# Performance work log

Measured on AMD Instinct MI355X. Metric: run time of the kernel, lower is better.

The kernel has to match this reference:

```python
import jax, jax.numpy as jnp
import numpy as np

B, SEG, DIM = 8, 16, 1024  # H = W = D = SEG is forced by the Linear(dim, dim) on H*S etc.
HID = DIM // 4


def setup_inputs() -> dict:
    key = jax.random.key(0)
    ks = jax.random.split(key, 16)
    def lin(k, i, o):
        return jax.random.normal(k, (i, o), jnp.float32) * 0.02
    return {
        "x": jax.random.normal(ks[0], (B, SEG, SEG, SEG, DIM), jnp.float32),
        "wh": lin(ks[1], DIM, DIM), "bh": jnp.zeros((DIM,), jnp.float32),
        "ww": lin(ks[2], DIM, DIM), "bw": jnp.zeros((DIM,), jnp.float32),
        "wd": lin(ks[3], DIM, DIM), "bd": jnp.zeros((DIM,), jnp.float32),
        "wc": lin(ks[4], DIM, DIM), "bc": jnp.zeros((DIM,), jnp.float32),
        "w1": lin(ks[5], DIM, HID), "b1": jnp.zeros((HID,), jnp.float32),
        "w2": lin(ks[6], HID, 4 * DIM), "b2": jnp.zeros((4 * DIM,), jnp.float32),
        "wp": lin(ks[7], DIM, DIM), "bp": jnp.zeros((DIM,), jnp.float32),
    }


def reference(x, wh, bh, ww, bw, wd, bd, wc, bc, w1, b1, w2, b2, wp, bp):
    Bn, H, Wn, D, C = x.shape
    seg = SEG
    S = C // seg
    xr = x.reshape(Bn, H, Wn, D, seg, S)

    # h-branch: mix along H axis (H*S == C)
    h = xr.transpose(0, 4, 2, 3, 1, 5).reshape(Bn, seg, Wn, D, H * S)
    h = (h @ wh + bh).reshape(Bn, seg, Wn, D, H, S).transpose(0, 4, 2, 3, 1, 5).reshape(Bn, H, Wn, D, C)

    # w-branch: mix along W axis
    w = xr.transpose(0, 1, 4, 3, 2, 5).reshape(Bn, H, seg, D, Wn * S)
    w = (w @ ww + bw).reshape(Bn, H, seg, D, Wn, S).transpose(0, 1, 4, 3, 2, 5).reshape(Bn, H, Wn, D, C)

    # d-branch: mix along D axis
    d = xr.transpose(0, 1, 2, 4, 3, 5).reshape(Bn, H, Wn, seg, D * S)
    d = (d @ wd + bd).reshape(Bn, H, Wn, seg, D, S).transpose(0, 1, 2, 4, 3, 5).reshape(Bn, H, Wn, D, C)

    # c-branch: plain channel mixing
    c = x @ wc + bc

    # reweight gate: global-average-pool then small MLP -> softmax over the 4 branches
    a = (h + w + d + c).mean(axis=(1, 2, 3))                 # (B, C)
    a = jax.nn.gelu(a @ w1 + b1, approximate=False) @ w2 + b2  # (B, 4C)
    a = jax.nn.softmax(a.reshape(Bn, C, 4).transpose(2, 0, 1), axis=0)  # (4, B, C)
    a = a[:, :, None, None, None, :]                          # (4, B, 1, 1, 1, C)

    out = h * a[0] + w * a[1] + d * a[2] + c * a[3]
    return out @ wp + bp
```

## Files before the change

kernel.cpp:

```cpp
#include <hip/hip_runtime.h>
#include <cstdint>
#include <cstddef>

typedef unsigned short u16;
typedef __attribute__((ext_vector_type(8))) __bf16 bf16x8;
typedef __attribute__((ext_vector_type(4))) float f32x4;
typedef __attribute__((ext_vector_type(4))) unsigned int u32x4;

__device__ __forceinline__ float bf2f(u16 u){
  union { unsigned int i; float f; } x; x.i = ((unsigned int)u) << 16; return x.f;
}
__device__ __forceinline__ u16 f2bf(float f){
  union { float f; unsigned int i; } x; x.f = f;
  unsigned int i = x.i;
  return (u16)((i + 0x7fffu + ((i >> 16) & 1u)) >> 16);
}
__device__ __forceinline__ void load_lds16(const u16* g, u16* l){
  __builtin_amdgcn_global_load_lds((const __attribute__((address_space(1))) void*)g,
                                   (__attribute__((address_space(3))) void*)l, 16, 0, 0);
}

__global__ __launch_bounds__(256) void k_transpose(
    const float* __restrict__ wh, const float* __restrict__ ww,
    const float* __restrict__ wd, const float* __restrict__ wc,
    const float* __restrict__ wp, u16* __restrict__ wT)
{
  __shared__ u16 tile[32][33];
  const float* src = (blockIdx.z==0)?wh:(blockIdx.z==1)?ww:(blockIdx.z==2)?wd:(blockIdx.z==3)?wc:wp;
  u16* dst = wT + (size_t)blockIdx.z * 1048576;
  int x = blockIdx.x*32 + threadIdx.x;
  int y0 = blockIdx.y*32;
  for (int i = threadIdx.y; i < 32; i += 8)
    tile[i][threadIdx.x] = f2bf(src[(size_t)(y0+i)*1024 + x]);
  __syncthreads();
  int x2 = y0 + threadIdx.x;
  int y2 = blockIdx.x*32;
  for (int i = threadIdx.y; i < 32; i += 8)
    dst[(size_t)(y2+i)*1024 + x2] = tile[threadIdx.x][i];
}

__global__ __launch_bounds__(256) void k_psum(
    const float* __restrict__ x, u16* __restrict__ xbf, float* __restrict__ P_h,
    float* __restrict__ PwP, float* __restrict__ PdP)
{
  const int b = blockIdx.x, cs = blockIdx.y, hg = blockIdx.z;
  const int th = threadIdx.x >> 7, tc = threadIdx.x & 127;
  const int h = hg*2 + th, c = cs*128 + tc;
  const size_t base = ((size_t)b<<22) + ((size_t)h<<18) + c;
  const float* xb = x + base;
  u16* xo = xbf + base;
  float sh = 0.f;
  float aW[16] = {}, aD[16] = {};
#pragma unroll
  for (int w = 0; w < 16; ++w)
#pragma unroll
    for (int d = 0; d < 16; ++d){
      float v = xb[(w<<14) + (d<<10)];
      xo[(w<<14) + (d<<10)] = f2bf(v);
      sh += v; aW[w] += v; aD[d] += v;
    }
  P_h[(size_t)((b<<4)+h)*1024 + c] = sh;
  const int part = hg*2 + th;
  float* pw = PwP + ((size_t)part<<17) + ((size_t)b<<14) + c;
  float* pd = PdP + ((size_t)part<<17) + ((size_t)b<<14) + c;
#pragma unroll
  for (int w = 0; w < 16; ++w) pw[w<<10] = aW[w];
#pragma unroll
  for (int d = 0; d < 16; ++d) pd[d<<10] = aD[d];
}

__global__ __launch_bounds__(256) void k_psum2(
    const float* __restrict__ PwP, const float* __restrict__ PdP,
    float* __restrict__ P_w, float* __restrict__ P_d)
{
  int idx = blockIdx.x*256 + threadIdx.x;
  float s = 0.f, t = 0.f;
#pragma unroll
  for (int p = 0; p < 16; ++p){ s += PwP[(size_t)p*131072 + idx]; t += PdP[(size_t)p*131072 + idx]; }
  P_w[idx] = s; P_d[idx] = t;
}

__global__ __launch_bounds__(256) void k_wred(
    const float* __restrict__ wh, const float* __restrict__ ww, const float* __restrict__ wd,
    float* __restrict__ wred)
{
  const float* src = (blockIdx.y==0)?wh:(blockIdx.y==1)?ww:wd;
  int idx = blockIdx.x*256 + threadIdx.x;
  int k = idx >> 6, S = idx & 63;
  float s = 0.f;
#pragma unroll
  for (int i = 0; i < 16; ++i) s += src[(size_t)k*1024 + i*64 + S];
  wred[(size_t)blockIdx.y*65536 + idx] = s;
}

__global__ __launch_bounds__(256) void k_asum(
    const float* __restrict__ P_h, const float* __restrict__ P_w, const float* __restrict__ P_d,
    const float* __restrict__ wred, const float* __restrict__ wc,
    const float* __restrict__ bhv, const float* __restrict__ bwv,
    const float* __restrict__ bdv, const float* __restrict__ bcv,
    float* __restrict__ a_sum)
{
  const int b = blockIdx.x, cs = blockIdx.y, tid = threadIdx.x;
  const int tc = tid & 127, ti = tid >> 7;
  const int c = cs*128 + tc, sg = c >> 6, S = c & 63;
  __shared__ float xbar[1024];
  __shared__ float red[2][128];
  for (int k = tid; k < 1024; k += 256){
    float s = 0.f;
#pragma unroll
    for (int hh = 0; hh < 16; ++hh) s += P_h[(size_t)(b*16+hh)*1024 + k];
    xbar[k] = s;
  }
  __syncthreads();
  const float* Ph = P_h + (size_t)b*16384;
  const float* Pw = P_w + (size_t)b*16384;
  const float* Pd = P_d + (size_t)b*16384;
  const float* whr = wred, *wwr = wred + 65536, *wdr = wred + 131072;
  float acc = 0.f;
  for (int i = ti*8; i < ti*8 + 8; ++i){
#pragma unroll 8
    for (int si = 0; si < 64; ++si){
      int k = i*64 + si;
      acc += Ph[i*1024 + sg*64 + si] * whr[(size_t)k*64 + S]
           + Pw[i*1024 + sg*64 + si] * wwr[(size_t)k*64 + S]
           + Pd[i*1024 + sg*64 + si] * wdr[(size_t)k*64 + S];
    }
  }
#pragma unroll 8
  for (int k = ti*512; k < ti*512 + 512; ++k) acc += xbar[k] * wc[(size_t)k*1024 + c];
  red[ti][tc] = acc;
  __syncthreads();
  if (ti == 0){
    float bs = 0.f;
#pragma unroll
    for (int i = 0; i < 16; ++i) bs += bhv[i*64+S] + bwv[i*64+S] + bdv[i*64+S];
    a_sum[b*1024 + c] = red[0][tc] + red[1][tc] + 4096.f*bcv[c] + 256.f*bs;
  }
}

__global__ __launch_bounds__(256) void k_mlp1(
    const float* __restrict__ a_sum, const float* __restrict__ w1,
    const float* __restrict__ b1, float* __restrict__ z1g)
{
  const int b = blockIdx.x, tid = threadIdx.x;
  __shared__ float af[1024];
  for (int i = tid; i < 1024; i += 256) af[i] = a_sum[b*1024 + i] * (1.0f/4096.0f);
  __syncthreads();
  float acc = b1[tid];
#pragma unroll 8
  for (int k = 0; k < 1024; ++k) acc += af[k] * w1[(size_t)k*256 + tid];
  z1g[b*256 + tid] = 0.5f * acc * (1.0f + erff(acc * 0.70710678118654752f));
}

__global__ __launch_bounds__(128) void k_mlp2(
    const float* __restrict__ z1g, const float* __restrict__ w2,
    const float* __restrict__ b2, float* __restrict__ alpha)
{
  const int b = blockIdx.x, js = blockIdx.y, tid = threadIdx.x;
  __shared__ float z1[256];
  z1[tid] = z1g[b*256 + tid];
  z1[tid+128] = z1g[b*256 + tid + 128];
  __syncthreads();
  const int cch = js*128 + tid;
  const int j0 = cch*4;
  f32x4 acc = *(const f32x4*)(b2 + j0);
#pragma unroll 8
  for (int k = 0; k < 256; ++k){
    f32x4 wv4 = *(const f32x4*)(w2 + (size_t)k*4096 + j0);
    float z = z1[k];
    acc[0] += z*wv4[0]; acc[1] += z*wv4[1]; acc[2] += z*wv4[2]; acc[3] += z*wv4[3];
  }
  float m = fmaxf(fmaxf(acc[0], acc[1]), fmaxf(acc[2], acc[3]));
  float e0 = expf(acc[0]-m), e1 = expf(acc[1]-m), e2 = expf(acc[2]-m), e3 = expf(acc[3]-m);
  float inv = 1.0f / (e0+e1+e2+e3);
  alpha[0*8192 + b*1024 + cch] = e0*inv;
  alpha[1*8192 + b*1024 + cch] = e1*inv;
  alpha[2*8192 + b*1024 + cch] = e2*inv;
  alpha[3*8192 + b*1024 + cch] = e3*inv;
}


#define STAGE_A(buf, kk, kt) \
  load_lds16(gA0 + (size_t)(kt)*strideK + (kk)*32, sA + (buf)*16384 + (kk)*8192); \
  load_lds16(gA1 + (size_t)(kt)*strideK + (kk)*32, sA + (buf)*16384 + (kk)*8192 + 4096)
#define STAGE_B(buf, kk, kt) \
  load_lds16(gB0 + (kt)*64 + (kk)*32, sB + (buf)*16384 + (kk)*8192); \
  load_lds16(gB1 + (kt)*64 + (kk)*32, sB + (buf)*16384 + (kk)*8192 + 4096)

#define PHASE(h, kk, buf, STAGE_STMT, VM) do{ \
  const u16* ar_ = ldsA + (buf)*16384 + (kk)*8192 + ardoff + (h)*2048; \
  const u16* br_ = ldsB + (buf)*16384 + (kk)*8192 + brdoff; \
  bf16x8 af_[4], bf_[4]; \
  _Pragma("unroll") for (int m_ = 0; m_ < 4; ++m_) af_[m_] = *(const bf16x8*)(ar_ + m_*512); \
  _Pragma("unroll") for (int n_ = 0; n_ < 4; ++n_) bf_[n_] = *(const bf16x8*)(br_ + n_*512); \
  STAGE_STMT; \
  if (VM) asm volatile("s_waitcnt vmcnt(4)" ::: "memory"); \
  __builtin_amdgcn_s_barrier(); \
  asm volatile("s_waitcnt lgkmcnt(0)" ::: "memory"); \
  __builtin_amdgcn_sched_barrier(0); \
  __builtin_amdgcn_s_setprio(1); \
  _Pragma("unroll") for (int m_ = 0; m_ < 4; ++m_) \
    _Pragma("unroll") for (int n_ = 0; n_ < 4; ++n_) \
      acc[(h)*4+m_][n_] = __builtin_amdgcn_mfma_f32_16x16x32_bf16(af_[m_], bf_[n_], acc[(h)*4+m_][n_], 0, 0, 0); \
  __builtin_amdgcn_s_setprio(0); \
  __builtin_amdgcn_s_barrier(); \
}while(0)

#define GEMM_PROLOGUE() do{ \
  load_lds16(gA0, sA);                 load_lds16(gA1, sA + 4096); \
  load_lds16(gB0, sB);                 load_lds16(gB1, sB + 4096); \
  load_lds16(gA0 + 32, sA + 8192);     load_lds16(gA1 + 32, sA + 8192 + 4096); \
  load_lds16(gB0 + 32, sB + 8192);     load_lds16(gB1 + 32, sB + 8192 + 4096); \
  load_lds16(gA0 + strideK, sA + 16384);   load_lds16(gA1 + strideK, sA + 16384 + 4096); \
  load_lds16(gB0 + 64, sB + 16384);        load_lds16(gB1 + 64, sB + 16384 + 4096); \
  asm volatile("s_waitcnt vmcnt(4)" ::: "memory"); \
  __builtin_amdgcn_s_barrier(); \
}while(0)

#define GEMM_MAINLOOP() \
  for (int i = 0; i < 8; ++i){ \
    const int t1 = 2*i + 1; \
    const int t2 = (2*i + 2 < 16) ? 2*i + 2 : 15; \
    const int t3 = (2*i + 3 < 16) ? 2*i + 3 : 15; \
    PHASE(0,0,0, STAGE_A(1,1,t1), 0); \
    PHASE(1,0,0, STAGE_B(1,1,t1), 0); \
    PHASE(0,1,0, STAGE_A(0,0,t2), 0); \
    PHASE(1,1,0, STAGE_B(0,0,t2), 1); \
    PHASE(0,0,1, STAGE_A(0,1,t2), 0); \
    PHASE(1,0,1, STAGE_B(0,1,t2), 0); \
    PHASE(0,1,1, STAGE_A(1,0,t3), 0); \
    PHASE(1,1,1, STAGE_B(1,0,t3), 1); \
  }

__global__ __launch_bounds__(512, 2) void k_branch_gemm(
    const u16* __restrict__ xbf, const u16* __restrict__ wT,
    const float* __restrict__ bh, const float* __restrict__ bw,
    const float* __restrict__ bd, const float* __restrict__ bc,
    u16* __restrict__ hbuf, u16* __restrict__ wbuf,
    u16* __restrict__ dbuf, u16* __restrict__ cbuf)
{
  const int p = blockIdx.x;
  const int id = (p & 7) * 256 + (p >> 3);
  const int ntile  = id & 3;
  const int rtile  = (id >> 2) & 127;
  const int branch = id >> 9;

  const int tid = threadIdx.x;
  const int wv = tid >> 6, l = tid & 63;

  __shared__ __align__(16) u16 ldsA[32768];
  __shared__ __align__(16) u16 ldsB[32768];

  const u16* wsel = wT + (size_t)branch * 1048576;
  const float* bias = (branch==0)?bh:(branch==1)?bw:(branch==2)?bd:bc;
  u16* obuf         = (branch==0)?hbuf:(branch==1)?wbuf:(branch==2)?dbuf:cbuf;

  const int lr = l >> 2;
  const int qg = ((l & 3) ^ ((lr >> 1) & 3)) * 8;
  int strideK;
  size_t cb0, cb1;
  {
    const int q1 = rtile & 15, b_ = rtile >> 4;
    const size_t q2a = wv, q2b = wv + 8;
    if (branch == 0){
      cb0 = ((size_t)b_<<22) + (q2a<<14) + ((size_t)q1<<6);
      cb1 = ((size_t)b_<<22) + (q2b<<14) + ((size_t)q1<<6);
      strideK = 262144;
    } else if (branch == 1){
      cb0 = ((size_t)b_<<22) + ((size_t)q1<<18) + (q2a<<6);
      cb1 = ((size_t)b_<<22) + ((size_t)q1<<18) + (q2b<<6);
      strideK = 16384;
    } else if (branch == 2){
      cb0 = ((size_t)b_<<22) + ((size_t)q1<<18) + (q2a<<14);
      cb1 = ((size_t)b_<<22) + ((size_t)q1<<18) + (q2b<<14);
      strideK = 1024;
    } else {
      size_t r0 = (size_t)(rtile*256 + wv*16);
      cb0 = r0 << 10; cb1 = (r0 + 128) << 10;
      strideK = 64;
    }
  }
  const int rsh = (branch == 2) ? 6 : 10;
  const u16* gA0 = xbf + cb0 + ((size_t)lr << rsh) + qg;
  const u16* gA1 = xbf + cb1 + ((size_t)lr << rsh) + qg;
  const u16* gB0 = wsel + (size_t)(ntile*256 + wv*16 + lr) * 1024 + qg;
  const u16* gB1 = gB0 + 128*1024;
  u16* sA = ldsA + wv*512;
  u16* sB = ldsB + wv*512;

  const int wm = wv >> 2, wn = wv & 3;
  const int fr = l & 15;
  const int cswz = ((l >> 4) ^ ((fr >> 1) & 3)) * 8;
  const int ardoff = (wm*128 + fr)*32 + cswz;
  const int brdoff = (wn*64  + fr)*32 + cswz;
  f32x4 acc[8][4] = {};

  GEMM_PROLOGUE();
  GEMM_MAINLOOP();

  const int bb_ = rtile >> 4, p1 = rtile & 15;
  int sc, s1, s2, s3;
  if      (branch==0){ sc=18; s1=6;  s2=14; s3=10; }
  else if (branch==1){ sc=14; s1=18; s2=6;  s3=10; }
  else if (branch==2){ sc=10; s1=18; s2=14; s3=6;  }
  else               { sc=6;  s1=18; s2=14; s3=10; }
#pragma unroll
  for (int mg = 0; mg < 8; ++mg){
    const int p2 = wm*8 + mg;
#pragma unroll
    for (int nf = 0; nf < 4; ++nf){
      int col = ntile*256 + wn*64 + nf*16 + fr;
      int ch = col >> 6, cl = col & 63;
      float bv = bias[col];
      size_t base = ((size_t)bb_<<22) | ((size_t)p1<<s1) | ((size_t)ch<<sc)
                  | ((size_t)p2<<s2) | (size_t)cl;
#pragma unroll
      for (int rg = 0; rg < 4; ++rg){
        int p3 = (l>>4)*4 + rg;
        obuf[base + ((size_t)p3<<s3)] = f2bf(acc[mg][nf][rg] + bv);
      }
    }
  }
}

__global__ __launch_bounds__(256) void k_mix(
    const u16* __restrict__ hbuf, const u16* __restrict__ wbuf,
    const u16* __restrict__ dbuf, const u16* __restrict__ cbuf,
    u16* __restrict__ mix, const float* __restrict__ alpha)
{
  int idx = blockIdx.x*256 + threadIdx.x;
  int p  = idx >> 7;
  int c0 = (idx & 127) << 3;
  int b = p >> 12;
  size_t off = ((size_t)p << 10) + c0;
  union { u32x4 v; u16 u[8]; } hv, wv, dv, cv, mv;
  hv.v = *(const u32x4*)(hbuf + off);
  wv.v = *(const u32x4*)(wbuf + off);
  dv.v = *(const u32x4*)(dbuf + off);
  cv.v = *(const u32x4*)(cbuf + off);
  union { f32x4 f[2]; float a[8]; } a0, a1, a2, a3;
  const float* ab = alpha + b*1024 + c0;
  a0.f[0] = *(const f32x4*)(ab);         a0.f[1] = *(const f32x4*)(ab + 4);
  a1.f[0] = *(const f32x4*)(ab + 8192);  a1.f[1] = *(const f32x4*)(ab + 8196);
  a2.f[0] = *(const f32x4*)(ab + 16384); a2.f[1] = *(const f32x4*)(ab + 16388);
  a3.f[0] = *(const f32x4*)(ab + 24576); a3.f[1] = *(const f32x4*)(ab + 24580);
#pragma unroll
  for (int e = 0; e < 8; ++e){
    float m = a0.a[e]*bf2f(hv.u[e]) + a1.a[e]*bf2f(wv.u[e])
            + a2.a[e]*bf2f(dv.u[e]) + a3.a[e]*bf2f(cv.u[e]);
    mv.u[e] = f2bf(m);
  }
  *(u32x4*)(mix + off) = mv.v;
}

__global__ __launch_bounds__(512, 2) void k_final_gemm(
    const u16* __restrict__ A, const u16* __restrict__ wpT,
    const float* __restrict__ bp, float* __restrict__ out)
{
  const int p = blockIdx.x;
  const int id = (p & 7) * 64 + (p >> 3);
  const int ntile = id & 3;
  const int rtile = id >> 2;

  const int tid = threadIdx.x;
  const int wv = tid >> 6, l = tid & 63;

  __shared__ __align__(16) u16 ldsA[32768];
  __shared__ __align__(16) u16 ldsB[32768];

  const int lr = l >> 2;
  const int qg = ((l & 3) ^ ((lr >> 1) & 3)) * 8;
  const int strideK = 64;
  const size_t r0 = (size_t)(rtile*256 + wv*16);
  const u16* gA0 = A + (r0 << 10) + ((size_t)lr << 10) + qg;
  const u16* gA1 = A + ((r0 + 128) << 10) + ((size_t)lr << 10) + qg;
  const u16* gB0 = wpT + (size_t)(ntile*256 + wv*16 + lr) * 1024 + qg;
  const u16* gB1 = gB0 + 128*1024;
  u16* sA = ldsA + wv*512;
  u16* sB = ldsB + wv*512;

  const int wm = wv >> 2, wn = wv & 3;
  const int fr = l & 15;
  const int cswz = ((l >> 4) ^ ((fr >> 1) & 3)) * 8;
  const int ardoff = (wm*128 + fr)*32 + cswz;
  const int brdoff = (wn*64  + fr)*32 + cswz;
  f32x4 acc[8][4] = {};

  GEMM_PROLOGUE();
  GEMM_MAINLOOP();

#pragma unroll
  for (int mg = 0; mg < 8; ++mg)
#pragma unroll
    for (int nf = 0; nf < 4; ++nf){
      int col = ntile*256 + wn*64 + nf*16 + fr;
      float bv = bp[col];
      int row0 = rtile*256 + wm*128 + mg*16 + (l>>4)*4;
#pragma unroll
      for (int rg = 0; rg < 4; ++rg)
        out[(size_t)(row0+rg)*1024 + col] = acc[mg][nf][rg] + bv;
    }
}

extern "C" void kernel_launch(void* const* d_in, const int* in_sizes, int n_in,
                              void* d_out, int out_size, void* d_ws, size_t ws_size,
                              hipStream_t stream)
{
  const float* x  = (const float*)d_in[0];
  const float* wh = (const float*)d_in[1];
  const float* bh = (const float*)d_in[2];
  const float* ww = (const float*)d_in[3];
  const float* bw = (const float*)d_in[4];
  const float* wd = (const float*)d_in[5];
  const float* bd = (const float*)d_in[6];
  const float* wc = (const float*)d_in[7];
  const float* bc = (const float*)d_in[8];
  const float* w1 = (const float*)d_in[9];
  const float* b1 = (const float*)d_in[10];
  const float* w2 = (const float*)d_in[11];
  const float* b2 = (const float*)d_in[12];
  const float* wp = (const float*)d_in[13];
  const float* bp = (const float*)d_in[14];
  char* ws = (char*)d_ws;
  char* ob = (char*)d_out;

  u16*   xbf   = (u16*)(ws);
  u16*   hbuf  = (u16*)(ws + 67108864);
  u16*   wbuf  = (u16*)(ws + 134217728);
  u16*   wT    = (u16*)(ws + 201326592);
  float* a_sum = (float*)(ws + 211812352);
  float* alpha = (float*)(ws + 211845120);
  float* z1g   = (float*)(ws + 211976192);
  u16*   mixb  = xbf;

  float* PwP  = (float*)(ob);
  float* PdP  = (float*)(ob + 8388608);
  float* P_h  = (float*)(ob + 16777216);
  float* P_w  = (float*)(ob + 17301504);
  float* P_d  = (float*)(ob + 17825792);
  float* wred = (float*)(ob + 18350080);
  u16*   cbuf = (u16*)ob;
  u16*   dbuf = (u16*)(ob + 67108864);
  float* outp = (float*)d_out;

  k_transpose  <<<dim3(32, 32, 5), dim3(32, 8), 0, stream>>>(wh, ww, wd, wc, wp, wT);
  k_psum       <<<dim3(8, 8, 8),   256, 0, stream>>>(x, xbf, P_h, PwP, PdP);
  k_psum2      <<<dim3(512),       256, 0, stream>>>(PwP, PdP, P_w, P_d);
  k_wred       <<<dim3(256, 3),    256, 0, stream>>>(wh, ww, wd, wred);
  k_asum       <<<dim3(8, 8),      256, 0, stream>>>(P_h, P_w, P_d, wred, wc, bh, bw, bd, bc, a_sum);
  k_mlp1       <<<dim3(8),         256, 0, stream>>>(a_sum, w1, b1, z1g);
  k_mlp2       <<<dim3(8, 8),      128, 0, stream>>>(z1g, w2, b2, alpha);
  k_branch_gemm<<<dim3(2048),      512, 0, stream>>>(xbf, wT, bh, bw, bd, bc,
                                                     hbuf, wbuf, dbuf, cbuf);
  k_mix        <<<dim3(16384),     256, 0, stream>>>(hbuf, wbuf, dbuf, cbuf, mixb, alpha);
  k_final_gemm <<<dim3(512),       512, 0, stream>>>(mixb, wT + 4*1048576, bp, outp);
  (void)in_sizes; (void)n_in; (void)out_size; (void)ws_size;
}
```

Measured before the change: 938.9 us.

## Make branch and final GEMMs persistent, prefetching next tile during epilogue

Both GEMM kernels become persistent-style. The branch GEMM launches 256 blocks, each looping over 8 row tiles; the final GEMM launches 256 blocks, each covering 2 column tiles. The first K stages of the next tile are issued before the current tile's epilogue stores, so the global-to-LDS loads overlap the output writes, and the last main-loop iteration is peeled to drain with vmcnt(0). This targets the prologue and epilogue bubbles of many short-lived blocks, at the cost of lower block-level parallelism and a tail if the 256 blocks do not fill the GPU evenly.

After: 997.8 us. 6.3% more time.

```diff
diff --git a/kernel.cpp b/kernel.cpp
--- a/kernel.cpp
+++ b/kernel.cpp
@@ -194,7 +194,8 @@
   _Pragma("unroll") for (int m_ = 0; m_ < 4; ++m_) af_[m_] = *(const bf16x8*)(ar_ + m_*512); \
   _Pragma("unroll") for (int n_ = 0; n_ < 4; ++n_) bf_[n_] = *(const bf16x8*)(br_ + n_*512); \
   STAGE_STMT; \
-  if (VM) asm volatile("s_waitcnt vmcnt(4)" ::: "memory"); \
+  if (VM == 1) asm volatile("s_waitcnt vmcnt(4)" ::: "memory"); \
+  if (VM == 2) asm volatile("s_waitcnt vmcnt(0)" ::: "memory"); \
   __builtin_amdgcn_s_barrier(); \
   asm volatile("s_waitcnt lgkmcnt(0)" ::: "memory"); \
   __builtin_amdgcn_sched_barrier(0); \
@@ -206,22 +207,18 @@
   __builtin_amdgcn_s_barrier(); \
 }while(0)
 
-#define GEMM_PROLOGUE() do{ \
+#define STAGE12() do{ \
   load_lds16(gA0, sA);                 load_lds16(gA1, sA + 4096); \
   load_lds16(gB0, sB);                 load_lds16(gB1, sB + 4096); \
   load_lds16(gA0 + 32, sA + 8192);     load_lds16(gA1 + 32, sA + 8192 + 4096); \
   load_lds16(gB0 + 32, sB + 8192);     load_lds16(gB1 + 32, sB + 8192 + 4096); \
   load_lds16(gA0 + strideK, sA + 16384);   load_lds16(gA1 + strideK, sA + 16384 + 4096); \
   load_lds16(gB0 + 64, sB + 16384);        load_lds16(gB1 + 64, sB + 16384 + 4096); \
-  asm volatile("s_waitcnt vmcnt(4)" ::: "memory"); \
-  __builtin_amdgcn_s_barrier(); \
 }while(0)
 
-#define GEMM_MAINLOOP() \
-  for (int i = 0; i < 8; ++i){ \
-    const int t1 = 2*i + 1; \
-    const int t2 = (2*i + 2 < 16) ? 2*i + 2 : 15; \
-    const int t3 = (2*i + 3 < 16) ? 2*i + 3 : 15; \
+#define GEMM_ITERS06() \
+  for (int i = 0; i < 7; ++i){ \
+    const int t1 = 2*i + 1, t2 = 2*i + 2, t3 = 2*i + 3; \
     PHASE(0,0,0, STAGE_A(1,1,t1), 0); \
     PHASE(1,0,0, STAGE_B(1,1,t1), 0); \
     PHASE(0,1,0, STAGE_A(0,0,t2), 0); \
@@ -232,6 +229,29 @@
     PHASE(1,1,1, STAGE_B(1,0,t3), 1); \
   }
 
+#define GEMM_ITER7() \
+  PHASE(0,0,0, STAGE_A(1,1,15), 0); \
+  PHASE(1,0,0, STAGE_B(1,1,15), 0); \
+  PHASE(0,1,0, (void)0, 0); \
+  PHASE(1,1,0, (void)0, 2); \
+  PHASE(0,0,1, (void)0, 0); \
+  PHASE(1,0,1, (void)0, 0); \
+  PHASE(0,1,1, (void)0, 0); \
+  PHASE(1,1,1, (void)0, 0);
+
+__device__ __forceinline__ void branch_abase(int branch, int rtile, int wv,
+                                             size_t& cb0, size_t& cb1){
+  const int q1 = rtile & 15, b_ = rtile >> 4;
+  const size_t q2a = wv, q2b = wv + 8;
+  if      (branch == 0){ cb0 = ((size_t)b_<<22) + (q2a<<14) + ((size_t)q1<<6);
+                         cb1 = ((size_t)b_<<22) + (q2b<<14) + ((size_t)q1<<6); }
+  else if (branch == 1){ cb0 = ((size_t)b_<<22) + ((size_t)q1<<18) + (q2a<<6);
+                         cb1 = ((size_t)b_<<22) + ((size_t)q1<<18) + (q2b<<6); }
+  else if (branch == 2){ cb0 = ((size_t)b_<<22) + ((size_t)q1<<18) + (q2a<<14);
+                         cb1 = ((size_t)b_<<22) + ((size_t)q1<<18) + (q2b<<14); }
+  else { size_t r0 = (size_t)(rtile*256 + wv*16); cb0 = r0 << 10; cb1 = (r0+128) << 10; }
+}
+
 __global__ __launch_bounds__(512, 2) void k_branch_gemm(
     const u16* __restrict__ xbf, const u16* __restrict__ wT,
     const float* __restrict__ bh, const float* __restrict__ bw,
@@ -240,10 +260,10 @@
     u16* __restrict__ dbuf, u16* __restrict__ cbuf)
 {
   const int p = blockIdx.x;
-  const int id = (p & 7) * 256 + (p >> 3);
-  const int ntile  = id & 3;
-  const int rtile  = (id >> 2) & 127;
-  const int branch = id >> 9;
+  const int xcd = p & 7, slot = p >> 3;
+  const int id0 = xcd*256 + slot;
+  const int ntile  = id0 & 3;
+  const int branch = id0 >> 9;
 
   const int tid = threadIdx.x;
   const int wv = tid >> 6, l = tid & 63;
@@ -257,32 +277,9 @@
 
   const int lr = l >> 2;
   const int qg = ((l & 3) ^ ((lr >> 1) & 3)) * 8;
-  int strideK;
-  size_t cb0, cb1;
-  {
-    const int q1 = rtile & 15, b_ = rtile >> 4;
-    const size_t q2a = wv, q2b = wv + 8;
-    if (branch == 0){
-      cb0 = ((size_t)b_<<22) + (q2a<<14) + ((size_t)q1<<6);
-      cb1 = ((size_t)b_<<22) + (q2b<<14) + ((size_t)q1<<6);
-      strideK = 262144;
-    } else if (branch == 1){
-      cb0 = ((size_t)b_<<22) + ((size_t)q1<<18) + (q2a<<6);
-      cb1 = ((size_t)b_<<22) + ((size_t)q1<<18) + (q2b<<6);
-      strideK = 16384;
-    } else if (branch == 2){
-      cb0 = ((size_t)b_<<22) + ((size_t)q1<<18) + (q2a<<14);
-      cb1 = ((size_t)b_<<22) + ((size_t)q1<<18) + (q2b<<14);
-      strideK = 1024;
-    } else {
-      size_t r0 = (size_t)(rtile*256 + wv*16);
-      cb0 = r0 << 10; cb1 = (r0 + 128) << 10;
-      strideK = 64;
-    }
-  }
+  const int strideK = (branch==0)?262144:(branch==1)?16384:(branch==2)?1024:64;
   const int rsh = (branch == 2) ? 6 : 10;
-  const u16* gA0 = xbf + cb0 + ((size_t)lr << rsh) + qg;
-  const u16* gA1 = xbf + cb1 + ((size_t)lr << rsh) + qg;
+
   const u16* gB0 = wsel + (size_t)(ntile*256 + wv*16 + lr) * 1024 + qg;
   const u16* gB1 = gB0 + 128*1024;
   u16* sA = ldsA + wv*512;
@@ -293,31 +290,56 @@
   const int cswz = ((l >> 4) ^ ((fr >> 1) & 3)) * 8;
   const int ardoff = (wm*128 + fr)*32 + cswz;
   const int brdoff = (wn*64  + fr)*32 + cswz;
-  f32x4 acc[8][4] = {};
-
-  GEMM_PROLOGUE();
-  GEMM_MAINLOOP();
-
-  const int bb_ = rtile >> 4, p1 = rtile & 15;
+
+  float bv4[4];
+#pragma unroll
+  for (int nf = 0; nf < 4; ++nf) bv4[nf] = bias[ntile*256 + wn*64 + nf*16 + fr];
   int sc, s1, s2, s3;
   if      (branch==0){ sc=18; s1=6;  s2=14; s3=10; }
   else if (branch==1){ sc=14; s1=18; s2=6;  s3=10; }
   else if (branch==2){ sc=10; s1=18; s2=14; s3=6;  }
   else               { sc=6;  s1=18; s2=14; s3=10; }
-#pragma unroll
-  for (int mg = 0; mg < 8; ++mg){
-    const int p2 = wm*8 + mg;
-#pragma unroll
-    for (int nf = 0; nf < 4; ++nf){
-      int col = ntile*256 + wn*64 + nf*16 + fr;
-      int ch = col >> 6, cl = col & 63;
-      float bv = bias[col];
-      size_t base = ((size_t)bb_<<22) | ((size_t)p1<<s1) | ((size_t)ch<<sc)
-                  | ((size_t)p2<<s2) | (size_t)cl;
-#pragma unroll
-      for (int rg = 0; rg < 4; ++rg){
-        int p3 = (l>>4)*4 + rg;
-        obuf[base + ((size_t)p3<<s3)] = f2bf(acc[mg][nf][rg] + bv);
+
+  int rtile = (id0 >> 2) & 127;
+  size_t cb0, cb1;
+  branch_abase(branch, rtile, wv, cb0, cb1);
+  const u16* gA0 = xbf + cb0 + ((size_t)lr << rsh) + qg;
+  const u16* gA1 = xbf + cb1 + ((size_t)lr << rsh) + qg;
+  STAGE12();
+  asm volatile("s_waitcnt vmcnt(4)" ::: "memory");
+  __builtin_amdgcn_s_barrier();
+
+  for (int j = 0; j < 8; ++j){
+    if (j){
+      asm volatile("s_waitcnt vmcnt(4)" ::: "memory");
+      __builtin_amdgcn_s_barrier();
+    }
+    f32x4 acc[8][4] = {};
+    GEMM_ITERS06();
+    GEMM_ITER7();
+    const int rtile_cur = rtile;
+    if (j < 7){
+      rtile = ((id0 + (j+1)*32) >> 2) & 127;
+      branch_abase(branch, rtile, wv, cb0, cb1);
+      gA0 = xbf + cb0 + ((size_t)lr << rsh) + qg;
+      gA1 = xbf + cb1 + ((size_t)lr << rsh) + qg;
+      STAGE12();
+    }
+    const int bb_ = rtile_cur >> 4, p1 = rtile_cur & 15;
+#pragma unroll
+    for (int mg = 0; mg < 8; ++mg){
+      const int p2 = wm*8 + mg;
+#pragma unroll
+      for (int nf = 0; nf < 4; ++nf){
+        int col = ntile*256 + wn*64 + nf*16 + fr;
+        int ch = col >> 6, cl = col & 63;
+        size_t base = ((size_t)bb_<<22) | ((size_t)p1<<s1) | ((size_t)ch<<sc)
+                    | ((size_t)p2<<s2) | (size_t)cl;
+#pragma unroll
+        for (int rg = 0; rg < 4; ++rg){
+          int p3 = (l>>4)*4 + rg;
+          obuf[base + ((size_t)p3<<s3)] = f2bf(acc[mg][nf][rg] + bv4[nf]);
+        }
       }
     }
   }
@@ -358,9 +380,9 @@
     const float* __restrict__ bp, float* __restrict__ out)
 {
   const int p = blockIdx.x;
-  const int id = (p & 7) * 64 + (p >> 3);
-  const int ntile = id & 3;
-  const int rtile = id >> 2;
+  const int xcd = p & 7, slot = p >> 3;
+  const int id0 = xcd*64 + slot*2;
+  const int rtile = id0 >> 2;
 
   const int tid = threadIdx.x;
   const int wv = tid >> 6, l = tid & 63;
@@ -374,6 +396,7 @@
   const size_t r0 = (size_t)(rtile*256 + wv*16);
   const u16* gA0 = A + (r0 << 10) + ((size_t)lr << 10) + qg;
   const u16* gA1 = A + ((r0 + 128) << 10) + ((size_t)lr << 10) + qg;
+  int ntile = id0 & 3;
   const u16* gB0 = wpT + (size_t)(ntile*256 + wv*16 + lr) * 1024 + qg;
   const u16* gB1 = gB0 + 128*1024;
   u16* sA = ldsA + wv*512;
@@ -384,22 +407,38 @@
   const int cswz = ((l >> 4) ^ ((fr >> 1) & 3)) * 8;
   const int ardoff = (wm*128 + fr)*32 + cswz;
   const int brdoff = (wn*64  + fr)*32 + cswz;
-  f32x4 acc[8][4] = {};
-
-  GEMM_PROLOGUE();
-  GEMM_MAINLOOP();
-
-#pragma unroll
-  for (int mg = 0; mg < 8; ++mg)
-#pragma unroll
-    for (int nf = 0; nf < 4; ++nf){
-      int col = ntile*256 + wn*64 + nf*16 + fr;
-      float bv = bp[col];
-      int row0 = rtile*256 + wm*128 + mg*16 + (l>>4)*4;
-#pragma unroll
-      for (int rg = 0; rg < 4; ++rg)
-        out[(size_t)(row0+rg)*1024 + col] = acc[mg][nf][rg] + bv;
-    }
+
+  STAGE12();
+  asm volatile("s_waitcnt vmcnt(4)" ::: "memory");
+  __builtin_amdgcn_s_barrier();
+
+  for (int j = 0; j < 2; ++j){
+    if (j){
+      asm volatile("s_waitcnt vmcnt(4)" ::: "memory");
+      __builtin_amdgcn_s_barrier();
+    }
+    f32x4 acc[8][4] = {};
+    GEMM_ITERS06();
+    GEMM_ITER7();
+    const int ntile_cur = ntile;
+    if (j < 1){
+      ntile = (id0 + 1) & 3;
+      gB0 = wpT + (size_t)(ntile*256 + wv*16 + lr) * 1024 + qg;
+      gB1 = gB0 + 128*1024;
+      STAGE12();
+    }
+#pragma unroll
+    for (int mg = 0; mg < 8; ++mg)
+#pragma unroll
+      for (int nf = 0; nf < 4; ++nf){
+        int col = ntile_cur*256 + wn*64 + nf*16 + fr;
+        float bv = bp[col];
+        int row0 = rtile*256 + wm*128 + mg*16 + (l>>4)*4;
+#pragma unroll
+        for (int rg = 0; rg < 4; ++rg)
+          out[(size_t)(row0+rg)*1024 + col] = acc[mg][nf][rg] + bv;
+      }
+  }
 }
 
 extern "C" void kernel_launch(void* const* d_in, const int* in_sizes, int n_in,
@@ -450,9 +489,9 @@
   k_asum       <<<dim3(8, 8),      256, 0, stream>>>(P_h, P_w, P_d, wred, wc, bh, bw, bd, bc, a_sum);
   k_mlp1       <<<dim3(8),         256, 0, stream>>>(a_sum, w1, b1, z1g);
   k_mlp2       <<<dim3(8, 8),      128, 0, stream>>>(z1g, w2, b2, alpha);
-  k_branch_gemm<<<dim3(2048),      512, 0, stream>>>(xbf, wT, bh, bw, bd, bc,
+  k_branch_gemm<<<dim3(256),       512, 0, stream>>>(xbf, wT, bh, bw, bd, bc,
                                                      hbuf, wbuf, dbuf, cbuf);
   k_mix        <<<dim3(16384),     256, 0, stream>>>(hbuf, wbuf, dbuf, cbuf, mixb, alpha);
-  k_final_gemm <<<dim3(512),       512, 0, stream>>>(mixb, wT + 4*1048576, bp, outp);
+  k_final_gemm <<<dim3(256),       512, 0, stream>>>(mixb, wT + 4*1048576, bp, outp);
   (void)in_sizes; (void)n_in; (void)out_size; (void)ws_size;
 }
```

## Merge GEMM half-phases into full-tile phases and split MLP1 reduction across threads

Applied to the files above, without the earlier changes.

The branch GEMM main loop now runs four phases per iteration instead of eight. Each phase loads all eight A fragments, issues 32 MFMAs, and stages both A and B for the next slice, which halves the barrier count. The final iteration is peeled so it stops issuing redundant prefetches and drains with vmcnt(0). It also splits the k-reduction of the tiny MLP1 kernel across 1024 threads with an LDS partial-sum step, which should cut its serial latency. The cost is more fragment registers live per phase and less interleaving of loads with compute inside each phase.

Result: faster. 896.5 us (-4.5%).

```diff
diff --git a/kernel.cpp b/kernel.cpp
--- a/kernel.cpp
+++ b/kernel.cpp
@@ -138,18 +138,25 @@
   }
 }
 
-__global__ __launch_bounds__(256) void k_mlp1(
+__global__ __launch_bounds__(1024) void k_mlp1(
     const float* __restrict__ a_sum, const float* __restrict__ w1,
     const float* __restrict__ b1, float* __restrict__ z1g)
 {
   const int b = blockIdx.x, tid = threadIdx.x;
+  const int j = tid & 255, ks = tid >> 8;
   __shared__ float af[1024];
-  for (int i = tid; i < 1024; i += 256) af[i] = a_sum[b*1024 + i] * (1.0f/4096.0f);
-  __syncthreads();
-  float acc = b1[tid];
+  __shared__ float part[4][256];
+  af[tid] = a_sum[b*1024 + tid] * (1.0f/4096.0f);
+  __syncthreads();
+  float acc = 0.f;
 #pragma unroll 8
-  for (int k = 0; k < 1024; ++k) acc += af[k] * w1[(size_t)k*256 + tid];
-  z1g[b*256 + tid] = 0.5f * acc * (1.0f + erff(acc * 0.70710678118654752f));
+  for (int k = ks*256; k < ks*256 + 256; ++k) acc += af[k] * w1[(size_t)k*256 + j];
+  part[ks][j] = acc;
+  __syncthreads();
+  if (ks == 0){
+    float a = part[0][j] + part[1][j] + part[2][j] + part[3][j] + b1[j];
+    z1g[b*256 + j] = 0.5f * a * (1.0f + erff(a * 0.70710678118654752f));
+  }
 }
 
 __global__ __launch_bounds__(128) void k_mlp2(
@@ -186,22 +193,29 @@
 #define STAGE_B(buf, kk, kt) \
   load_lds16(gB0 + (kt)*64 + (kk)*32, sB + (buf)*16384 + (kk)*8192); \
   load_lds16(gB1 + (kt)*64 + (kk)*32, sB + (buf)*16384 + (kk)*8192 + 4096)
-
-#define PHASE(h, kk, buf, STAGE_STMT, VM) do{ \
-  const u16* ar_ = ldsA + (buf)*16384 + (kk)*8192 + ardoff + (h)*2048; \
+#define STAGE_AB(buf, kk, kt) STAGE_A(buf, kk, kt); STAGE_B(buf, kk, kt)
+
+#define MPHASE(kk, buf, STAGE_STMT, VM) do{ \
+  const u16* ar_ = ldsA + (buf)*16384 + (kk)*8192 + ardoff; \
   const u16* br_ = ldsB + (buf)*16384 + (kk)*8192 + brdoff; \
-  bf16x8 af_[4], bf_[4]; \
-  _Pragma("unroll") for (int m_ = 0; m_ < 4; ++m_) af_[m_] = *(const bf16x8*)(ar_ + m_*512); \
+  bf16x8 af_[8], bf_[4]; \
+  _Pragma("unroll") for (int m_ = 0; m_ < 4; ++m_){ \
+    af_[m_]   = *(const bf16x8*)(ar_ + m_*512); \
+    af_[4+m_] = *(const bf16x8*)(ar_ + 2048 + m_*512); \
+  } \
   _Pragma("unroll") for (int n_ = 0; n_ < 4; ++n_) bf_[n_] = *(const bf16x8*)(br_ + n_*512); \
   STAGE_STMT; \
-  if (VM) asm volatile("s_waitcnt vmcnt(4)" ::: "memory"); \
+  if (VM == 1) asm volatile("s_waitcnt vmcnt(4)" ::: "memory"); \
+  if (VM == 2) asm volatile("s_waitcnt vmcnt(0)" ::: "memory"); \
   __builtin_amdgcn_s_barrier(); \
   asm volatile("s_waitcnt lgkmcnt(0)" ::: "memory"); \
   __builtin_amdgcn_sched_barrier(0); \
   __builtin_amdgcn_s_setprio(1); \
   _Pragma("unroll") for (int m_ = 0; m_ < 4; ++m_) \
-    _Pragma("unroll") for (int n_ = 0; n_ < 4; ++n_) \
-      acc[(h)*4+m_][n_] = __builtin_amdgcn_mfma_f32_16x16x32_bf16(af_[m_], bf_[n_], acc[(h)*4+m_][n_], 0, 0, 0); \
+    _Pragma("unroll") for (int n_ = 0; n_ < 4; ++n_){ \
+      acc[m_][n_]   = __builtin_amdgcn_mfma_f32_16x16x32_bf16(af_[m_],   bf_[n_], acc[m_][n_],   0, 0, 0); \
+      acc[4+m_][n_] = __builtin_amdgcn_mfma_f32_16x16x32_bf16(af_[4+m_], bf_[n_], acc[4+m_][n_], 0, 0, 0); \
+    } \
   __builtin_amdgcn_s_setprio(0); \
   __builtin_amdgcn_s_barrier(); \
 }while(0)
@@ -218,19 +232,17 @@
 }while(0)
 
 #define GEMM_MAINLOOP() \
-  for (int i = 0; i < 8; ++i){ \
-    const int t1 = 2*i + 1; \
-    const int t2 = (2*i + 2 < 16) ? 2*i + 2 : 15; \
-    const int t3 = (2*i + 3 < 16) ? 2*i + 3 : 15; \
-    PHASE(0,0,0, STAGE_A(1,1,t1), 0); \
-    PHASE(1,0,0, STAGE_B(1,1,t1), 0); \
-    PHASE(0,1,0, STAGE_A(0,0,t2), 0); \
-    PHASE(1,1,0, STAGE_B(0,0,t2), 1); \
-    PHASE(0,0,1, STAGE_A(0,1,t2), 0); \
-    PHASE(1,0,1, STAGE_B(0,1,t2), 0); \
-    PHASE(0,1,1, STAGE_A(1,0,t3), 0); \
-    PHASE(1,1,1, STAGE_B(1,0,t3), 1); \
-  }
+  for (int i = 0; i < 7; ++i){ \
+    const int t1 = 2*i + 1, t2 = 2*i + 2, t3 = 2*i + 3; \
+    MPHASE(0,0, STAGE_AB(1,1,t1), 0); \
+    MPHASE(1,0, STAGE_AB(0,0,t2), 1); \
+    MPHASE(0,1, STAGE_AB(0,1,t2), 0); \
+    MPHASE(1,1, STAGE_AB(1,0,t3), 1); \
+  } \
+  MPHASE(0,0, STAGE_AB(1,1,15), 0); \
+  MPHASE(1,0, (void)0, 2); \
+  MPHASE(0,1, (void)0, 0); \
+  MPHASE(1,1, (void)0, 0);
 
 __global__ __launch_bounds__(512, 2) void k_branch_gemm(
     const u16* __restrict__ xbf, const u16* __restrict__ wT,
@@ -448,7 +460,7 @@
   k_psum2      <<<dim3(512),       256, 0, stream>>>(PwP, PdP, P_w, P_d);
   k_wred       <<<dim3(256, 3),    256, 0, stream>>>(wh, ww, wd, wred);
   k_asum       <<<dim3(8, 8),      256, 0, stream>>>(P_h, P_w, P_d, wred, wc, bh, bw, bd, bc, a_sum);
-  k_mlp1       <<<dim3(8),         256, 0, stream>>>(a_sum, w1, b1, z1g);
+  k_mlp1       <<<dim3(8),         1024, 0, stream>>>(a_sum, w1, b1, z1g);
   k_mlp2       <<<dim3(8, 8),      128, 0, stream>>>(z1g, w2, b2, alpha);
   k_branch_gemm<<<dim3(2048),      512, 0, stream>>>(xbf, wT, bh, bw, bd, bc,
                                                      hbuf, wbuf, dbuf, cbuf);
```
